# Kernel optimization log

Hardware: AMD Instinct MI355X
Metric: run time of the kernel (lower is better)

Reference implementation:

```python
import jax, jax.numpy as jnp
import numpy as np

B, N, D = 32768, 20, 13  # batch, n_humans, rotated-state dim (last input channel is mask)
LAYERS = {
    'm1': [(D, 150), (150, 100)],          # mlp1, last_relu=True
    'm2': [(100, 100), (100, 50)],          # mlp2
    'at': [(200, 100), (100, 100), (100, 1)],  # attention (global state concat -> 2*100 in)
    'hp': [(100, 100), (100, 100), (100, 7)],  # human_state_predictor (50*2 in)
}

def _mlp(x, params, last_relu=False):
    n = len(params)
    for i, (W, b) in enumerate(params):
        x = x @ W + b
        if i < n - 1 or last_relu:
            x = jax.nn.relu(x)
    return x

def setup_inputs() -> dict:
    key = jax.random.key(0)
    ks, kx, km = jax.random.split(key, 3)
    inp = {}
    for name, shapes in LAYERS.items():
        for i, (fi, fo) in enumerate(shapes):
            kw, kb, ks = jax.random.split(jax.random.fold_in(ks, i), 3)
            inp[f'{name}_w{i}'] = jax.random.normal(kw, (fi, fo), jnp.float32) / jnp.sqrt(float(fi))
            inp[f'{name}_b{i}'] = jnp.zeros((fo,), jnp.float32)
    x = jax.random.normal(kx, (B, N, D + 1), jnp.float32)
    mask = (jax.random.uniform(km, (B, N)) < 0.9).astype(jnp.float32)  # 0/1 visibility mask
    inp['state'] = x.at[..., -1].set(mask)
    return inp

def reference(state, m1_w0, m1_b0, m1_w1, m1_b1,
              m2_w0, m2_b0, m2_w1, m2_b1,
              at_w0, at_b0, at_w1, at_b1, at_w2, at_b2,
              hp_w0, hp_b0, hp_w1, hp_b1, hp_w2, hp_b2):
    x, mask = state[..., :-1], state[..., -1]        # (B,N,D), (B,N)
    h1 = _mlp(x, [(m1_w0, m1_b0), (m1_w1, m1_b1)], last_relu=True)   # (B,N,100)
    h2 = _mlp(h1, [(m2_w0, m2_b0), (m2_w1, m2_b1)])                   # (B,N,50)

    # masked mean-pool global state (NaN-on-empty zeroed, as in torch)
    msum = jnp.sum(mask, axis=1, keepdims=True)                       # (B,1)
    mw = jnp.where(msum > 0, mask / jnp.where(msum > 0, msum, 1.0), 0.0)
    global_state = jnp.sum(mw[..., None] * h1, axis=1, keepdims=True) # (B,1,100)
    att_in = jnp.concatenate([h1, jnp.broadcast_to(global_state, h1.shape)], axis=-1)

    scores = _mlp(att_in, [(at_w0, at_b0), (at_w1, at_b1), (at_w2, at_b2)])[..., 0]  # (B,N)
    scores = scores * mask
    se = jnp.exp(scores) * (scores != 0).astype(scores.dtype)
    ssum = jnp.sum(se, axis=1, keepdims=True)
    w = jnp.where(ssum > 0, se / jnp.where(ssum > 0, ssum, 1.0), 0.0)[..., None]  # (B,N,1)

    wsum = jnp.sum(w * h2, axis=1, keepdims=True)                     # (B,1,50)
    joint = jnp.concatenate([h2, jnp.broadcast_to(wsum, h2.shape)], axis=-1)  # (B,N,100)
    return _mlp(joint, [(hp_w0, hp_b0), (hp_w1, hp_b1), (hp_w2, hp_b2)])      # (B,N,7)
```

## Files before the change

### kernel.cpp

```cpp
#include <hip/hip_runtime.h>
#include <hip/hip_bf16.h>


typedef short sx8 __attribute__((ext_vector_type(8)));
typedef short sx4 __attribute__((ext_vector_type(4)));
typedef float fx4 __attribute__((ext_vector_type(4)));
typedef unsigned ux2 __attribute__((ext_vector_type(2)));

#define TB   512
#define NW   8
#define NB   4
#define MTOK 80
#define MT   5
#define CHH  640
#define CHG  128

#define OFF_BUFT 0
#define OFF_BUFA 25600
#define OFF_BUFH 46080
#define OFF_BUFG 56320
#define OFF_BIAS 60416
#define OFF_GRC  63808
#define OFF_WRC  65600
#define OFF_SC   67392
#define OFF_MASK 67712
#define OFF_MSUM 68032
#define OFF_WTM  68048
#define SMEM_BYTES 71120

#define B_M1B0 0
#define B_M1B1 152
#define B_M2B0 256
#define B_M2B1 360
#define B_ATB0 416
#define B_ATB1 520
#define B_HPB0 624
#define B_HPB1 728
#define B_HPB2 832

#define WS_M1W0  0
#define WS_M1W1  5120
#define WS_M2W0  23040
#define WS_M2W1  37376
#define WS_ATW0  45568
#define WS_ATW1  59904
#define WS_HPW0  74240
#define WS_HPW1  81408
#define WS_HPW2  95744
#define WS_ATW0H 97792
#define WS_HPW0H 112128
#define WS_ATW2  119296

__device__ __forceinline__ short f2b(float f) {
    unsigned u = __builtin_bit_cast(unsigned, f);
    u += 0x7FFFu + ((u >> 16) & 1u);
    return (short)(u >> 16);
}
__device__ __forceinline__ float b2f(short h) {
    unsigned u = ((unsigned)(unsigned short)h) << 16;
    return __builtin_bit_cast(float, u);
}
__device__ __forceinline__ sx4 pack4(fx4 v) {
    __hip_bfloat162 lo = __float22bfloat162_rn(make_float2(v[0], v[1]));
    __hip_bfloat162 hi = __float22bfloat162_rn(make_float2(v[2], v[3]));
    ux2 p;
    unsigned ulo, uhi;
    __builtin_memcpy(&ulo, &lo, 4);
    __builtin_memcpy(&uhi, &hi, 4);
    p[0] = ulo; p[1] = uhi;
    return __builtin_bit_cast(sx4, p);
}

__device__ __forceinline__ void stg(const float* __restrict__ W, int N,
                                    int KR, int KPAD, int NR, int Nsrc,
                                    short* dst, int gtid, int gsz) {
    int K8 = KPAD >> 3;
    for (int idx = gtid; idx < NR * K8; idx += gsz) {
        int k8 = idx / NR, nl = idx - k8 * NR;
        int k0 = k8 << 3;
        sx8 h;
        #pragma unroll
        for (int i = 0; i < 8; ++i) {
            int k = k0 + i;
            float v = (k < KR && nl < Nsrc) ? W[k * N + nl] : 0.f;
            h[i] = f2b(v);
        }
        *(sx8*)(dst + (k8 * NR + nl) * 8) = h;
    }
}

__global__ void stage_weights(
    const float* __restrict__ m1w0, const float* __restrict__ m1w1,
    const float* __restrict__ m2w0, const float* __restrict__ m2w1,
    const float* __restrict__ atw0, const float* __restrict__ atw1,
    const float* __restrict__ hpw0, const float* __restrict__ hpw1,
    const float* __restrict__ hpw2, const float* __restrict__ atw2,
    short* __restrict__ ws)
{
    int gtid = blockIdx.x * blockDim.x + threadIdx.x;
    int gsz = gridDim.x * blockDim.x;
    stg(m1w0, 150, 13, 32, 160, 150, ws + WS_M1W0, gtid, gsz);
    stg(m1w1, 100, 150, 160, 112, 100, ws + WS_M1W1, gtid, gsz);
    stg(m2w0, 100, 100, 128, 112, 100, ws + WS_M2W0, gtid, gsz);
    stg(m2w1, 50, 100, 128, 64, 50, ws + WS_M2W1, gtid, gsz);
    stg(atw0, 100, 100, 128, 112, 100, ws + WS_ATW0, gtid, gsz);
    stg(atw1, 100, 100, 128, 112, 100, ws + WS_ATW1, gtid, gsz);
    stg(hpw0, 100, 50, 64, 112, 100, ws + WS_HPW0, gtid, gsz);
    stg(hpw1, 100, 100, 128, 112, 100, ws + WS_HPW1, gtid, gsz);
    stg(hpw2, 7, 100, 128, 16, 7, ws + WS_HPW2, gtid, gsz);
    stg(atw0 + 100 * 100, 100, 100, 128, 112, 100, ws + WS_ATW0H, gtid, gsz);
    stg(hpw0 + 50 * 100, 100, 50, 64, 112, 100, ws + WS_HPW0H, gtid, gsz);
    stg(atw2, 1, 100, 128, 16, 1, ws + WS_ATW2, gtid, gsz);
}

template <int KT, int NT, bool RELU, bool UINIT>
__device__ __forceinline__ void gemm(const short* __restrict__ wg, int NR,
                                     const short* bIn, short* bOut,
                                     const float* initp, int initBstride,
                                     int wave, int lm, int lq) {
    constexpr int NG = (NT + 1) / 2;
    for (int u = wave; u < NG * 3; u += NW) {
        int ng = u / 3, mg = u - ng * 3;
        int nt0 = ng * 2, nt1 = nt0 + 1;
        bool hasN1 = !((NT & 1) && (ng == NG - 1));
        sx8 a0[KT], a1[KT];
        #pragma unroll
        for (int kt = 0; kt < KT; ++kt)
            a0[kt] = *(const sx8*)(wg + ((kt * 4 + lq) * NR + nt0 * 16 + lm) * 8);
        if (hasN1) {
            #pragma unroll
            for (int kt = 0; kt < KT; ++kt)
                a1[kt] = *(const sx8*)(wg + ((kt * 4 + lq) * NR + nt1 * 16 + lm) * 8);
        }
        int n0l0 = nt0 * 16 + lq * 4;
        int n0l1 = nt1 * 16 + lq * 4;
        fx4 ib0, ib1;
        if (UINIT) {
            ib0 = *(const fx4*)(initp + n0l0);
            if (hasN1) ib1 = *(const fx4*)(initp + n0l1);
        }
        int mcount = (mg == 2) ? 1 : 2;
        #pragma unroll 2
        for (int mi = 0; mi < mcount; ++mi) {
            int mt = mg * 2 + mi;
            int tok = mt * 16 + lm;
            sx8 bfr[KT];
            #pragma unroll
            for (int kt = 0; kt < KT; ++kt)
                bfr[kt] = *(const sx8*)(bIn + (kt * 4 + lq) * CHH + tok * 8);
            fx4 acc0, acc1;
            if (UINIT) acc0 = ib0;
            else acc0 = *(const fx4*)(initp + (tok / 20) * initBstride + n0l0);
            if (hasN1) {
                if (UINIT) acc1 = ib1;
                else acc1 = *(const fx4*)(initp + (tok / 20) * initBstride + n0l1);
            }
            #pragma unroll
            for (int kt = 0; kt < KT; ++kt) {
                acc0 = __builtin_amdgcn_mfma_f32_16x16x32_bf16(a0[kt], bfr[kt], acc0, 0, 0, 0);
                if (hasN1)
                    acc1 = __builtin_amdgcn_mfma_f32_16x16x32_bf16(a1[kt], bfr[kt], acc1, 0, 0, 0);
            }
            if (RELU) {
                #pragma unroll
                for (int r = 0; r < 4; ++r) acc0[r] = fmaxf(acc0[r], 0.f);
            }
            *(sx4*)(bOut + (nt0 * 2 + (lq >> 1)) * CHH + tok * 8 + (lq & 1) * 4) = pack4(acc0);
            if (hasN1) {
                if (RELU) {
                    #pragma unroll
                    for (int r = 0; r < 4; ++r) acc1[r] = fmaxf(acc1[r], 0.f);
                }
                *(sx4*)(bOut + (nt1 * 2 + (lq >> 1)) * CHH + tok * 8 + (lq & 1) * 4) = pack4(acc1);
            }
        }
    }
}

template <int KT, int NT>
__device__ __forceinline__ void gemmR(const short* __restrict__ wg, int NR,
                                      const short* bG, float* outF,
                                      const float* biasp,
                                      int wave, int lm, int lq) {
    constexpr int NG = (NT + 1) / 2;
    for (int u = wave; u < NG; u += NW) {
        int nt0 = u * 2, nt1 = nt0 + 1;
        bool hasN1 = !((NT & 1) && (u == NG - 1));
        sx8 a0[KT], a1[KT], bfr[KT];
        #pragma unroll
        for (int kt = 0; kt < KT; ++kt) {
            a0[kt] = *(const sx8*)(wg + ((kt * 4 + lq) * NR + nt0 * 16 + lm) * 8);
            bfr[kt] = *(const sx8*)(bG + (kt * 4 + lq) * CHG + lm * 8);
        }
        if (hasN1) {
            #pragma unroll
            for (int kt = 0; kt < KT; ++kt)
                a1[kt] = *(const sx8*)(wg + ((kt * 4 + lq) * NR + nt1 * 16 + lm) * 8);
        }
        int n0l0 = nt0 * 16 + lq * 4;
        int n0l1 = nt1 * 16 + lq * 4;
        fx4 acc0 = *(const fx4*)(biasp + n0l0);
        fx4 acc1;
        if (hasN1) acc1 = *(const fx4*)(biasp + n0l1);
        #pragma unroll
        for (int kt = 0; kt < KT; ++kt) {
            acc0 = __builtin_amdgcn_mfma_f32_16x16x32_bf16(a0[kt], bfr[kt], acc0, 0, 0, 0);
            if (hasN1)
                acc1 = __builtin_amdgcn_mfma_f32_16x16x32_bf16(a1[kt], bfr[kt], acc1, 0, 0, 0);
        }
        if (lm < NB) {
            *(fx4*)(outF + lm * 112 + n0l0) = acc0;
            if (hasN1) *(fx4*)(outF + lm * 112 + n0l1) = acc1;
        }
    }
}

template <int NT>
__device__ __forceinline__ void gemmT(const short* __restrict__ act,
                                      const short* __restrict__ wT,
                                      short* __restrict__ bG,
                                      int wave, int lm, int lq) {
    for (int nt = wave; nt < NT; nt += NW) {
        int j = nt * 16 + lm;
        const short* ap = act + (j >> 3) * CHH + (j & 7);
        fx4 acc = {0.f, 0.f, 0.f, 0.f};
        #pragma unroll
        for (int kt = 0; kt < 3; ++kt) {
            int tok0 = kt * 32 + lq * 8;
            int tok0e = (tok0 < MTOK) ? tok0 : 0;
            sx8 a;
            #pragma unroll
            for (int i = 0; i < 8; ++i) {
                int ii = (i + lq * 2) & 7;
                a[i] = ap[(tok0e + ii) * 8];
            }
            sx8 b = *(const sx8*)(wT + lm * 96 + tok0);
            acc = __builtin_amdgcn_mfma_f32_16x16x32_bf16(a, b, acc, 0, 0, 0);
        }
        if (lm < NB) {
            *(sx4*)(bG + (nt * 2 + (lq >> 1)) * CHG + lm * 8 + (lq & 1) * 4) = pack4(acc);
        }
    }
}

__device__ __forceinline__ void zpad(short* buf, int tid) {
    for (int i = tid; i < 160; i += TB) {
        sx8 z = {0, 0, 0, 0, 0, 0, 0, 0};
        *(sx8*)(buf + 14 * CHH + i * 8) = z;
    }
}

__global__ __launch_bounds__(TB, 4) void sp_mfma_bf16(
    const float* __restrict__ state,
    const float* __restrict__ m1b0, const float* __restrict__ m1b1,
    const float* __restrict__ m2b0, const float* __restrict__ m2b1,
    const float* __restrict__ atb0, const float* __restrict__ atb1,
    const float* __restrict__ atb2,
    const float* __restrict__ hpb0, const float* __restrict__ hpb1,
    const float* __restrict__ hpb2,
    const short* __restrict__ ws,
    float* __restrict__ out)
{
    __shared__ __align__(16) unsigned char smem[SMEM_BYTES];
    short* bufT  = (short*)(smem + OFF_BUFT);
    short* bufA  = (short*)(smem + OFF_BUFA);
    short* bufH2 = (short*)(smem + OFF_BUFH);
    short* bufG  = (short*)(smem + OFF_BUFG);
    float* biasv = (float*)(smem + OFF_BIAS);
    float* grc   = (float*)(smem + OFF_GRC);
    float* wrc   = (float*)(smem + OFF_WRC);
    float* scv   = (float*)(smem + OFF_SC);
    float* maskv = (float*)(smem + OFF_MASK);
    float* msum  = (float*)(smem + OFF_MSUM);
    short* wTm   = (short*)(smem + OFF_WTM);

    const int tid  = threadIdx.x;
    const int lane = tid & 63;
    const int wave = tid >> 6;
    const int lm   = lane & 15;
    const int lq   = lane >> 4;
    const long gt0 = (long)blockIdx.x * MTOK;

    {
        const float* bs[9] = {m1b0, m1b1, m2b0, m2b1, atb0, atb1, hpb0, hpb1, hpb2};
        const int off[9] = {B_M1B0, B_M1B1, B_M2B0, B_M2B1, B_ATB0, B_ATB1, B_HPB0, B_HPB1, B_HPB2};
        const int sz[9]  = {150, 100, 100, 50, 100, 100, 100, 100, 7};
        const int pd[9]  = {152, 104, 104, 56, 104, 104, 104, 104, 16};
        #pragma unroll
        for (int r = 0; r < 9; ++r)
            for (int i = tid; i < pd[r]; i += TB)
                biasv[off[r] + i] = (i < sz[r]) ? bs[r][i] : 0.f;
        if (tid < MTOK) maskv[tid] = state[(gt0 + tid) * 14 + 13];
        for (int t = tid; t < 256; t += TB) {
            sx8 z = {0, 0, 0, 0, 0, 0, 0, 0};
            *(sx8*)(bufG + t * 8) = z;
        }
        for (int idx = tid; idx < MTOK * 4; idx += TB) {
            int row = idx >> 2, seg = idx & 3;
            const float* xp = state + (gt0 + row) * 14;
            sx8 h;
            #pragma unroll
            for (int i = 0; i < 8; ++i) {
                int k = seg * 8 + i;
                float v = (k < 13) ? xp[k] : 0.f;
                h[i] = f2b(v);
            }
            *(sx8*)(bufA + seg * CHH + row * 8) = h;
        }
    }
    __syncthreads();

    if (tid < NB) {
        float s = 0.f;
        #pragma unroll
        for (int n = 0; n < 20; ++n) s += maskv[tid * 20 + n];
        msum[tid] = s;
    }
    gemm<1, 10, true, true>(ws + WS_M1W0, 160, bufA, bufT, biasv + B_M1B0, 0,
                            wave, lm, lq);
    __syncthreads();

    gemm<5, 7, true, true>(ws + WS_M1W1, 112, bufT, bufA, biasv + B_M1B1, 0,
                           wave, lm, lq);
    zpad(bufA, tid);
    for (int t = tid; t < 1536; t += TB) {
        int b = t / 96, tp = t - b * 96;
        int tau = (tp & ~7) | ((tp + ((tp >> 3) & 3) * 2) & 7);
        float v = 0.f;
        if (b < NB && tau < MTOK && tau / 20 == b) {
            float ms = msum[b];
            v = (ms > 0.f) ? maskv[tau] / ms : 0.f;
        }
        wTm[t] = f2b(v);
    }
    __syncthreads();

    gemmT<7>(bufA, wTm, bufG, wave, lm, lq);
    gemm<4, 7, true, true>(ws + WS_M2W0, 112, bufA, bufT, biasv + B_M2B0, 0,
                           wave, lm, lq);
    zpad(bufT, tid);
    __syncthreads();

    gemmR<4, 7>(ws + WS_ATW0H, 112, bufG, grc, biasv + B_ATB0, wave, lm, lq);
    gemm<4, 4, false, true>(ws + WS_M2W1, 64, bufT, bufH2, biasv + B_M2B1, 0,
                            wave, lm, lq);
    __syncthreads();

    gemm<4, 7, true, false>(ws + WS_ATW0, 112, bufA, bufT, grc, 112,
                            wave, lm, lq);
    __syncthreads();

    gemm<4, 7, true, true>(ws + WS_ATW1, 112, bufT, bufA, biasv + B_ATB1, 0,
                           wave, lm, lq);
    __syncthreads();

    {
        float atb2s = atb2[0];
        sx8 afr[4];
        #pragma unroll
        for (int kt = 0; kt < 4; ++kt)
            afr[kt] = *(const sx8*)(ws + WS_ATW2 + ((kt * 4 + lq) * 16 + lm) * 8);
        for (int mt = wave; mt < MT; mt += NW) {
            int tok = mt * 16 + lm;
            fx4 acc = {0.f, 0.f, 0.f, 0.f};
            const short* bp = bufA + tok * 8;
            #pragma unroll
            for (int kt = 0; kt < 4; ++kt) {
                sx8 b = *(const sx8*)(bp + (kt * 4 + lq) * CHH);
                acc = __builtin_amdgcn_mfma_f32_16x16x32_bf16(afr[kt], b, acc, 0, 0, 0);
            }
            if (lq == 0) {
                float s = (acc[0] + atb2s) * maskv[tok];
                scv[tok] = (s != 0.f) ? __expf(s) : 0.f;
            }
        }
    }
    __syncthreads();

    for (int t = tid; t < 1536; t += TB) {
        int b = t / 96, tp = t - b * 96;
        int tau = (tp & ~7) | ((tp + ((tp >> 3) & 3) * 2) & 7);
        float v = 0.f;
        if (b < NB && tau < MTOK && tau / 20 == b) {
            float ss = 0.f;
            #pragma unroll
            for (int n = 0; n < 20; ++n) ss += scv[b * 20 + n];
            v = (ss > 0.f) ? scv[tau] / ss : 0.f;
        }
        wTm[t] = f2b(v);
    }
    __syncthreads();

    gemmT<4>(bufH2, wTm, bufG, wave, lm, lq);
    __syncthreads();

    gemmR<2, 7>(ws + WS_HPW0H, 112, bufG, wrc, biasv + B_HPB0, wave, lm, lq);
    __syncthreads();

    gemm<2, 7, true, false>(ws + WS_HPW0, 112, bufH2, bufT, wrc, 112,
                            wave, lm, lq);
    __syncthreads();

    gemm<4, 7, true, true>(ws + WS_HPW1, 112, bufT, bufA, biasv + B_HPB1, 0,
                           wave, lm, lq);
    __syncthreads();

    {
        sx8 afr[4];
        #pragma unroll
        for (int kt = 0; kt < 4; ++kt)
            afr[kt] = *(const sx8*)(ws + WS_HPW2 + ((kt * 4 + lq) * 16 + lm) * 8);
        fx4 ib = *(const fx4*)(biasv + B_HPB2 + lq * 4);
        for (int mt = wave; mt < MT; mt += NW) {
            int tok = mt * 16 + lm;
            fx4 acc = ib;
            const short* bp = bufA + tok * 8;
            #pragma unroll
            for (int kt = 0; kt < 4; ++kt) {
                sx8 b = *(const sx8*)(bp + (kt * 4 + lq) * CHH);
                acc = __builtin_amdgcn_mfma_f32_16x16x32_bf16(afr[kt], b, acc, 0, 0, 0);
            }
            #pragma unroll
            for (int r = 0; r < 4; ++r) {
                int n = lq * 4 + r;
                if (n < 7) out[(gt0 + tok) * 7 + n] = acc[r];
            }
        }
    }
}

extern "C" void kernel_launch(void* const* d_in, const int* in_sizes, int n_in,
                              void* d_out, int out_size, void* d_ws, size_t ws_size,
                              hipStream_t stream) {
    int si = 20, wb = 0;
    if (in_sizes[0] > 1000000) { si = 0; wb = 1; }
    const float* state = (const float*)d_in[si];
    const float* W[20];
    for (int i = 0; i < 20; ++i) W[i] = (const float*)d_in[wb + i];
    float* out = (float*)d_out;
    short* ws = (short*)d_ws;
    int Btot = in_sizes[si] / (20 * 14);
    int nblocks = Btot / NB;

    hipLaunchKernelGGL(stage_weights, dim3(128), dim3(256), 0, stream,
        W[0], W[2], W[4], W[6], W[8], W[10], W[14], W[16], W[18], W[12], ws);

    hipLaunchKernelGGL(sp_mfma_bf16, dim3(nblocks), dim3(TB), 0, stream,
        state,
        W[1], W[3],
        W[5], W[7],
        W[9], W[11],
        W[13],
        W[15], W[17], W[19],
        ws, out);
}
```

Baseline: 414.7 us.

## Assign one batch element per wave with private LDS regions, dropping block barriers

Restructures the fused MLP kernel so each of 4 waves owns one batch element (20 tokens) with its own LDS activation region, instead of 8 waves cooperatively tiling 80 tokens. Most layers now run wave-locally without __syncthreads, and the masked mean-pool and attention-weighted sum are computed with direct FMA loops rather than MFMA transposes through a staging matrix. Each wave computes two overlapping 16-token tiles (tokens 0-15 and 4-19), which duplicates some MFMA work, and launch bounds drop to 2 blocks of 256 threads per CU.

After: 484.9 us. +16.9%, slower.

```diff
diff --git a/kernel.cpp b/kernel.cpp
--- a/kernel.cpp
+++ b/kernel.cpp
@@ -7,26 +7,20 @@
 typedef float fx4 __attribute__((ext_vector_type(4)));
 typedef unsigned ux2 __attribute__((ext_vector_type(2)));
 
-#define TB   512
-#define NW   8
+#define TB   256
+#define NW   4
 #define NB   4
-#define MTOK 80
-#define MT   5
-#define CHH  640
+#define CHW  160
 #define CHG  128
-
-#define OFF_BUFT 0
-#define OFF_BUFA 25600
-#define OFF_BUFH 46080
+#define WREG 7040
+
+#define OFF_ACT  0
 #define OFF_BUFG 56320
 #define OFF_BIAS 60416
-#define OFF_GRC  63808
-#define OFF_WRC  65600
-#define OFF_SC   67392
-#define OFF_MASK 67712
-#define OFF_MSUM 68032
-#define OFF_WTM  68048
-#define SMEM_BYTES 71120
+#define OFF_RC   63808
+#define OFF_SC   65600
+#define OFF_MASK 65920
+#define SMEM_BYTES 66240
 
 #define B_M1B0 0
 #define B_M1B1 152
@@ -113,66 +107,34 @@
     stg(atw2, 1, 100, 128, 16, 1, ws + WS_ATW2, gtid, gsz);
 }
 
-template <int KT, int NT, bool RELU, bool UINIT>
-__device__ __forceinline__ void gemm(const short* __restrict__ wg, int NR,
-                                     const short* bIn, short* bOut,
-                                     const float* initp, int initBstride,
-                                     int wave, int lm, int lq) {
-    constexpr int NG = (NT + 1) / 2;
-    for (int u = wave; u < NG * 3; u += NW) {
-        int ng = u / 3, mg = u - ng * 3;
-        int nt0 = ng * 2, nt1 = nt0 + 1;
-        bool hasN1 = !((NT & 1) && (ng == NG - 1));
-        sx8 a0[KT], a1[KT];
+template <int KT, int NT, bool RELU>
+__device__ __forceinline__ void wgemm(const short* __restrict__ wg, int NR,
+                                      const short* bIn, short* bOut,
+                                      const float* initp, int lm, int lq) {
+    #pragma unroll 2
+    for (int nt = 0; nt < NT; ++nt) {
+        sx8 a[KT];
         #pragma unroll
         for (int kt = 0; kt < KT; ++kt)
-            a0[kt] = *(const sx8*)(wg + ((kt * 4 + lq) * NR + nt0 * 16 + lm) * 8);
-        if (hasN1) {
+            a[kt] = *(const sx8*)(wg + ((kt * 4 + lq) * NR + nt * 16 + lm) * 8);
+        int n0 = nt * 16 + lq * 4;
+        fx4 ib = *(const fx4*)(initp + n0);
+        #pragma unroll
+        for (int mt = 0; mt < 2; ++mt) {
+            int tok = (mt ? 4 : 0) + lm;
+            sx8 bfr[KT];
             #pragma unroll
             for (int kt = 0; kt < KT; ++kt)
-                a1[kt] = *(const sx8*)(wg + ((kt * 4 + lq) * NR + nt1 * 16 + lm) * 8);
-        }
-        int n0l0 = nt0 * 16 + lq * 4;
-        int n0l1 = nt1 * 16 + lq * 4;
-        fx4 ib0, ib1;
-        if (UINIT) {
-            ib0 = *(const fx4*)(initp + n0l0);
-            if (hasN1) ib1 = *(const fx4*)(initp + n0l1);
-        }
-        int mcount = (mg == 2) ? 1 : 2;
-        #pragma unroll 2
-        for (int mi = 0; mi < mcount; ++mi) {
-            int mt = mg * 2 + mi;
-            int tok = mt * 16 + lm;
-            sx8 bfr[KT];
+                bfr[kt] = *(const sx8*)(bIn + (kt * 4 + lq) * CHW + tok * 8);
+            fx4 acc = ib;
             #pragma unroll
             for (int kt = 0; kt < KT; ++kt)
-                bfr[kt] = *(const sx8*)(bIn + (kt * 4 + lq) * CHH + tok * 8);
-            fx4 acc0, acc1;
-            if (UINIT) acc0 = ib0;
-            else acc0 = *(const fx4*)(initp + (tok / 20) * initBstride + n0l0);
-            if (hasN1) {
-                if (UINIT) acc1 = ib1;
-                else acc1 = *(const fx4*)(initp + (tok / 20) * initBstride + n0l1);
-            }
-            #pragma unroll
-            for (int kt = 0; kt < KT; ++kt) {
-                acc0 = __builtin_amdgcn_mfma_f32_16x16x32_bf16(a0[kt], bfr[kt], acc0, 0, 0, 0);
-                if (hasN1)
-                    acc1 = __builtin_amdgcn_mfma_f32_16x16x32_bf16(a1[kt], bfr[kt], acc1, 0, 0, 0);
-            }
+                acc = __builtin_amdgcn_mfma_f32_16x16x32_bf16(a[kt], bfr[kt], acc, 0, 0, 0);
             if (RELU) {
                 #pragma unroll
-                for (int r = 0; r < 4; ++r) acc0[r] = fmaxf(acc0[r], 0.f);
-            }
-            *(sx4*)(bOut + (nt0 * 2 + (lq >> 1)) * CHH + tok * 8 + (lq & 1) * 4) = pack4(acc0);
-            if (hasN1) {
-                if (RELU) {
-                    #pragma unroll
-                    for (int r = 0; r < 4; ++r) acc1[r] = fmaxf(acc1[r], 0.f);
-                }
-                *(sx4*)(bOut + (nt1 * 2 + (lq >> 1)) * CHH + tok * 8 + (lq & 1) * 4) = pack4(acc1);
-            }
+                for (int r = 0; r < 4; ++r) acc[r] = fmaxf(acc[r], 0.f);
+            }
+            *(sx4*)(bOut + (nt * 2 + (lq >> 1)) * CHW + tok * 8 + (lq & 1) * 4) = pack4(acc);
         }
     }
 }
@@ -215,42 +177,13 @@
     }
 }
 
-template <int NT>
-__device__ __forceinline__ void gemmT(const short* __restrict__ act,
-                                      const short* __restrict__ wT,
-                                      short* __restrict__ bG,
-                                      int wave, int lm, int lq) {
-    for (int nt = wave; nt < NT; nt += NW) {
-        int j = nt * 16 + lm;
-        const short* ap = act + (j >> 3) * CHH + (j & 7);
-        fx4 acc = {0.f, 0.f, 0.f, 0.f};
-        #pragma unroll
-        for (int kt = 0; kt < 3; ++kt) {
-            int tok0 = kt * 32 + lq * 8;
-            int tok0e = (tok0 < MTOK) ? tok0 : 0;
-            sx8 a;
-            #pragma unroll
-            for (int i = 0; i < 8; ++i) {
-                int ii = (i + lq * 2) & 7;
-                a[i] = ap[(tok0e + ii) * 8];
-            }
-            sx8 b = *(const sx8*)(wT + lm * 96 + tok0);
-            acc = __builtin_amdgcn_mfma_f32_16x16x32_bf16(a, b, acc, 0, 0, 0);
-        }
-        if (lm < NB) {
-            *(sx4*)(bG + (nt * 2 + (lq >> 1)) * CHG + lm * 8 + (lq & 1) * 4) = pack4(acc);
-        }
-    }
-}
-
-__device__ __forceinline__ void zpad(short* buf, int tid) {
-    for (int i = tid; i < 160; i += TB) {
-        sx8 z = {0, 0, 0, 0, 0, 0, 0, 0};
-        *(sx8*)(buf + 14 * CHH + i * 8) = z;
-    }
-}
-
-__global__ __launch_bounds__(TB, 4) void sp_mfma_bf16(
+__device__ __forceinline__ void zpad2(short* rg, int lane) {
+    sx8 z = {0, 0, 0, 0, 0, 0, 0, 0};
+    for (int i = lane; i < 40; i += 64)
+        *(sx8*)(rg + 14 * CHW + i * 8) = z;
+}
+
+__global__ __launch_bounds__(TB, 2) void sp_wave_bf16(
     const float* __restrict__ state,
     const float* __restrict__ m1b0, const float* __restrict__ m1b1,
     const float* __restrict__ m2b0, const float* __restrict__ m2b1,
@@ -262,24 +195,24 @@
     float* __restrict__ out)
 {
     __shared__ __align__(16) unsigned char smem[SMEM_BYTES];
-    short* bufT  = (short*)(smem + OFF_BUFT);
-    short* bufA  = (short*)(smem + OFF_BUFA);
-    short* bufH2 = (short*)(smem + OFF_BUFH);
     short* bufG  = (short*)(smem + OFF_BUFG);
     float* biasv = (float*)(smem + OFF_BIAS);
-    float* grc   = (float*)(smem + OFF_GRC);
-    float* wrc   = (float*)(smem + OFF_WRC);
+    float* rc    = (float*)(smem + OFF_RC);
     float* scv   = (float*)(smem + OFF_SC);
     float* maskv = (float*)(smem + OFF_MASK);
-    float* msum  = (float*)(smem + OFF_MSUM);
-    short* wTm   = (short*)(smem + OFF_WTM);
 
     const int tid  = threadIdx.x;
     const int lane = tid & 63;
     const int wave = tid >> 6;
     const int lm   = lane & 15;
     const int lq   = lane >> 4;
-    const long gt0 = (long)blockIdx.x * MTOK;
+    const int b20  = wave * 20;
+    const long gt0 = (long)blockIdx.x * (NB * 20);
+
+    short* act = (short*)(smem + OFF_ACT) + wave * WREG;
+    short* R1 = act;
+    short* R2 = act + 3200;
+    short* R3 = act + 5760;
 
     {
         const float* bs[9] = {m1b0, m1b1, m2b0, m2b1, atb0, atb1, hpb0, hpb1, hpb2};
@@ -290,14 +223,16 @@
         for (int r = 0; r < 9; ++r)
             for (int i = tid; i < pd[r]; i += TB)
                 biasv[off[r] + i] = (i < sz[r]) ? bs[r][i] : 0.f;
-        if (tid < MTOK) maskv[tid] = state[(gt0 + tid) * 14 + 13];
-        for (int t = tid; t < 256; t += TB) {
-            sx8 z = {0, 0, 0, 0, 0, 0, 0, 0};
-            *(sx8*)(bufG + t * 8) = z;
-        }
-        for (int idx = tid; idx < MTOK * 4; idx += TB) {
+        sx8 z = {0, 0, 0, 0, 0, 0, 0, 0};
+        for (int t = tid; t < 192; t += TB) {
+            int k8 = t / 12, c = 4 + t - (t / 12) * 12;
+            *(sx8*)(bufG + (k8 * 16 + c) * 8) = z;
+        }
+        if (lane < 20)
+            maskv[b20 + lane] = state[(gt0 + b20 + lane) * 14 + 13];
+        for (int idx = lane; idx < 80; idx += 64) {
             int row = idx >> 2, seg = idx & 3;
-            const float* xp = state + (gt0 + row) * 14;
+            const float* xp = state + (gt0 + b20 + row) * 14;
             sx8 h;
             #pragma unroll
             for (int i = 0; i < 8; ++i) {
@@ -305,125 +240,112 @@
                 float v = (k < 13) ? xp[k] : 0.f;
                 h[i] = f2b(v);
             }
-            *(sx8*)(bufA + seg * CHH + row * 8) = h;
-        }
-    }
-    __syncthreads();
-
-    if (tid < NB) {
-        float s = 0.f;
-        #pragma unroll
-        for (int n = 0; n < 20; ++n) s += maskv[tid * 20 + n];
-        msum[tid] = s;
-    }
-    gemm<1, 10, true, true>(ws + WS_M1W0, 160, bufA, bufT, biasv + B_M1B0, 0,
-                            wave, lm, lq);
-    __syncthreads();
-
-    gemm<5, 7, true, true>(ws + WS_M1W1, 112, bufT, bufA, biasv + B_M1B1, 0,
-                           wave, lm, lq);
-    zpad(bufA, tid);
-    for (int t = tid; t < 1536; t += TB) {
-        int b = t / 96, tp = t - b * 96;
-        int tau = (tp & ~7) | ((tp + ((tp >> 3) & 3) * 2) & 7);
-        float v = 0.f;
-        if (b < NB && tau < MTOK && tau / 20 == b) {
-            float ms = msum[b];
-            v = (ms > 0.f) ? maskv[tau] / ms : 0.f;
-        }
-        wTm[t] = f2b(v);
-    }
-    __syncthreads();
-
-    gemmT<7>(bufA, wTm, bufG, wave, lm, lq);
-    gemm<4, 7, true, true>(ws + WS_M2W0, 112, bufA, bufT, biasv + B_M2B0, 0,
-                           wave, lm, lq);
-    zpad(bufT, tid);
-    __syncthreads();
-
-    gemmR<4, 7>(ws + WS_ATW0H, 112, bufG, grc, biasv + B_ATB0, wave, lm, lq);
-    gemm<4, 4, false, true>(ws + WS_M2W1, 64, bufT, bufH2, biasv + B_M2B1, 0,
-                            wave, lm, lq);
-    __syncthreads();
-
-    gemm<4, 7, true, false>(ws + WS_ATW0, 112, bufA, bufT, grc, 112,
-                            wave, lm, lq);
-    __syncthreads();
-
-    gemm<4, 7, true, true>(ws + WS_ATW1, 112, bufT, bufA, biasv + B_ATB1, 0,
-                           wave, lm, lq);
-    __syncthreads();
-
+            *(sx8*)(R3 + seg * CHW + row * 8) = h;
+        }
+    }
+    __syncthreads();
+
+    wgemm<1, 10, true>(ws + WS_M1W0, 160, R3, R1, biasv + B_M1B0, lm, lq);
+    wgemm<5, 7, true>(ws + WS_M1W1, 112, R1, R2, biasv + B_M1B1, lm, lq);
+    zpad2(R2, lane);
+    {
+        float ms = 0.f;
+        #pragma unroll
+        for (int t = 0; t < 20; ++t) ms += maskv[b20 + t];
+        float inv = (ms > 0.f) ? 1.f / ms : 0.f;
+        for (int j = lane; j < 128; j += 64) {
+            float g = 0.f;
+            if (j < 100) {
+                #pragma unroll
+                for (int t = 0; t < 20; ++t)
+                    g = fmaf(maskv[b20 + t],
+                             b2f(R2[(j >> 3) * CHW + t * 8 + (j & 7)]), g);
+                g *= inv;
+            }
+            bufG[(j >> 3) * CHG + wave * 8 + (j & 7)] = f2b(g);
+        }
+    }
+    wgemm<4, 7, true>(ws + WS_M2W0, 112, R2, R1, biasv + B_M2B0, lm, lq);
+    zpad2(R1, lane);
+    wgemm<4, 4, false>(ws + WS_M2W1, 64, R1, R3, biasv + B_M2B1, lm, lq);
+    __syncthreads();
+
+    gemmR<4, 7>(ws + WS_ATW0H, 112, bufG, rc, biasv + B_ATB0, wave, lm, lq);
+    __syncthreads();
+
+    wgemm<4, 7, true>(ws + WS_ATW0, 112, R2, R1, rc + wave * 112, lm, lq);
+    zpad2(R1, lane);
+    wgemm<4, 7, true>(ws + WS_ATW1, 112, R1, R2, biasv + B_ATB1, lm, lq);
+    zpad2(R2, lane);
     {
         float atb2s = atb2[0];
         sx8 afr[4];
         #pragma unroll
         for (int kt = 0; kt < 4; ++kt)
             afr[kt] = *(const sx8*)(ws + WS_ATW2 + ((kt * 4 + lq) * 16 + lm) * 8);
-        for (int mt = wave; mt < MT; mt += NW) {
-            int tok = mt * 16 + lm;
+        #pragma unroll
+        for (int mt = 0; mt < 2; ++mt) {
+            int tok = (mt ? 4 : 0) + lm;
             fx4 acc = {0.f, 0.f, 0.f, 0.f};
-            const short* bp = bufA + tok * 8;
+            const short* bp = R2 + tok * 8;
             #pragma unroll
             for (int kt = 0; kt < 4; ++kt) {
-                sx8 b = *(const sx8*)(bp + (kt * 4 + lq) * CHH);
+                sx8 b = *(const sx8*)(bp + (kt * 4 + lq) * CHW);
                 acc = __builtin_amdgcn_mfma_f32_16x16x32_bf16(afr[kt], b, acc, 0, 0, 0);
             }
             if (lq == 0) {
-                float s = (acc[0] + atb2s) * maskv[tok];
-                scv[tok] = (s != 0.f) ? __expf(s) : 0.f;
-            }
-        }
-    }
-    __syncthreads();
-
-    for (int t = tid; t < 1536; t += TB) {
-        int b = t / 96, tp = t - b * 96;
-        int tau = (tp & ~7) | ((tp + ((tp >> 3) & 3) * 2) & 7);
+                float s = (acc[0] + atb2s) * maskv[b20 + tok];
+                scv[b20 + tok] = (s != 0.f) ? __expf(s) : 0.f;
+            }
+        }
+    }
+    {
+        float ss = 0.f;
+        #pragma unroll
+        for (int t = 0; t < 20; ++t) ss += scv[b20 + t];
+        float inv = (ss > 0.f) ? 1.f / ss : 0.f;
+        int j = lane;
         float v = 0.f;
-        if (b < NB && tau < MTOK && tau / 20 == b) {
-            float ss = 0.f;
-            #pragma unroll
-            for (int n = 0; n < 20; ++n) ss += scv[b * 20 + n];
-            v = (ss > 0.f) ? scv[tau] / ss : 0.f;
-        }
-        wTm[t] = f2b(v);
-    }
-    __syncthreads();
-
-    gemmT<4>(bufH2, wTm, bufG, wave, lm, lq);
-    __syncthreads();
-
-    gemmR<2, 7>(ws + WS_HPW0H, 112, bufG, wrc, biasv + B_HPB0, wave, lm, lq);
-    __syncthreads();
-
-    gemm<2, 7, true, false>(ws + WS_HPW0, 112, bufH2, bufT, wrc, 112,
-                            wave, lm, lq);
-    __syncthreads();
-
-    gemm<4, 7, true, true>(ws + WS_HPW1, 112, bufT, bufA, biasv + B_HPB1, 0,
-                           wave, lm, lq);
-    __syncthreads();
-
+        if (j < 50) {
+            #pragma unroll
+            for (int t = 0; t < 20; ++t)
+                v = fmaf(scv[b20 + t],
+                         b2f(R3[(j >> 3) * CHW + t * 8 + (j & 7)]), v);
+            v *= inv;
+        }
+        bufG[(j >> 3) * CHG + wave * 8 + (j & 7)] = f2b(v);
+    }
+    __syncthreads();
+
+    gemmR<2, 7>(ws + WS_HPW0H, 112, bufG, rc, biasv + B_HPB0, wave, lm, lq);
+    __syncthreads();
+
+    wgemm<2, 7, true>(ws + WS_HPW0, 112, R3, R1, rc + wave * 112, lm, lq);
+    zpad2(R1, lane);
+    wgemm<4, 7, true>(ws + WS_HPW1, 112, R1, R2, biasv + B_HPB1, lm, lq);
+    zpad2(R2, lane);
     {
         sx8 afr[4];
         #pragma unroll
         for (int kt = 0; kt < 4; ++kt)
             afr[kt] = *(const sx8*)(ws + WS_HPW2 + ((kt * 4 + lq) * 16 + lm) * 8);
         fx4 ib = *(const fx4*)(biasv + B_HPB2 + lq * 4);
-        for (int mt = wave; mt < MT; mt += NW) {
-            int tok = mt * 16 + lm;
+        #pragma unroll
+        for (int mt = 0; mt < 2; ++mt) {
+            int tok = (mt ? 4 : 0) + lm;
             fx4 acc = ib;
-            const short* bp = bufA + tok * 8;
+            const short* bp = R2 + tok * 8;
             #pragma unroll
             for (int kt = 0; kt < 4; ++kt) {
-                sx8 b = *(const sx8*)(bp + (kt * 4 + lq) * CHH);
+                sx8 b = *(const sx8*)(bp + (kt * 4 + lq) * CHW);
                 acc = __builtin_amdgcn_mfma_f32_16x16x32_bf16(afr[kt], b, acc, 0, 0, 0);
             }
-            #pragma unroll
-            for (int r = 0; r < 4; ++r) {
-                int n = lq * 4 + r;
-                if (n < 7) out[(gt0 + tok) * 7 + n] = acc[r];
+            if (mt == 0 || lm >= 12) {
+                #pragma unroll
+                for (int r = 0; r < 4; ++r) {
+                    int n = lq * 4 + r;
+                    if (n < 7) out[(gt0 + b20 + tok) * 7 + n] = acc[r];
+                }
             }
         }
     }
@@ -445,7 +367,7 @@
     hipLaunchKernelGGL(stage_weights, dim3(128), dim3(256), 0, stream,
         W[0], W[2], W[4], W[6], W[8], W[10], W[14], W[16], W[18], W[12], ws);
 
-    hipLaunchKernelGGL(sp_mfma_bf16, dim3(nblocks), dim3(TB), 0, stream,
+    hipLaunchKernelGGL(sp_wave_bf16, dim3(nblocks), dim3(TB), 0, stream,
         state,
         W[1], W[3],
         W[5], W[7],
```
